# Optimization experiments

Hardware: AMD Instinct MI355X
Metric: run time of the kernel (lower is better)

## Reference

```python
import jax, jax.numpy as jnp
import numpy as np

DIM = 1024
HEADS = 16
HEAD_DIM = DIM // HEADS
HIDDEN = 4 * DIM
B, N = 2, 2048
LS_INIT = 1e-4


def _layernorm(x, w, b, eps=1e-5):
    mu = jnp.mean(x, axis=-1, keepdims=True)
    var = jnp.var(x, axis=-1, keepdims=True)
    return (x - mu) * jax.lax.rsqrt(var + eps) * w + b


def setup_inputs() -> dict:
    key = jax.random.key(0)
    ks = jax.random.split(key, 8)
    s = 0.02
    return {
        "x": jax.random.normal(ks[0], (B, N, DIM), jnp.float32),
        "ln1_w": jnp.ones((DIM,), jnp.float32),
        "ln1_b": jnp.zeros((DIM,), jnp.float32),
        "qkv_w": jax.random.normal(ks[1], (3 * DIM, DIM), jnp.float32) * s,
        "qkv_b": jnp.zeros((3 * DIM,), jnp.float32),
        "proj_w": jax.random.normal(ks[2], (DIM, DIM), jnp.float32) * s,
        "proj_b": jnp.zeros((DIM,), jnp.float32),
        "ls1_gamma": jnp.full((DIM,), LS_INIT, jnp.float32),
        "ln2_w": jnp.ones((DIM,), jnp.float32),
        "ln2_b": jnp.zeros((DIM,), jnp.float32),
        "fc1_w": jax.random.normal(ks[3], (HIDDEN, DIM), jnp.float32) * s,
        "fc1_b": jnp.zeros((HIDDEN,), jnp.float32),
        "fc2_w": jax.random.normal(ks[4], (DIM, HIDDEN), jnp.float32) * s,
        "fc2_b": jnp.zeros((DIM,), jnp.float32),
        "ls2_gamma": jnp.full((DIM,), LS_INIT, jnp.float32),
    }


def reference(x, ln1_w, ln1_b, qkv_w, qkv_b, proj_w, proj_b, ls1_gamma,
              ln2_w, ln2_b, fc1_w, fc1_b, fc2_w, fc2_b, ls2_gamma):
    Bn, Nn, C = x.shape
    scale = HEAD_DIM ** -0.5

    # --- attention branch (pre-norm) ---
    h = _layernorm(x, ln1_w, ln1_b)
    qkv = h @ qkv_w.T + qkv_b                      # [B,N,3C]
    qkv = qkv.reshape(Bn, Nn, 3, HEADS, HEAD_DIM)
    q = qkv[:, :, 0].transpose(0, 2, 1, 3)         # [B,H,N,D]
    k = qkv[:, :, 1].transpose(0, 2, 1, 3)
    v = qkv[:, :, 2].transpose(0, 2, 1, 3)
    attn = jnp.einsum('bhnd,bhmd->bhnm', q, k) * scale  # [B,H,N,N]
    attn = jax.nn.softmax(attn, axis=-1)
    o = jnp.einsum('bhnm,bhmd->bhnd', attn, v)
    o = o.transpose(0, 2, 1, 3).reshape(Bn, Nn, C)
    o = o @ proj_w.T + proj_b
    x = x + o * ls1_gamma

    # --- MLP branch (pre-norm) ---
    h = _layernorm(x, ln2_w, ln2_b)
    h = jax.nn.gelu(h @ fc1_w.T + fc1_b, approximate=False)
    h = h @ fc2_w.T + fc2_b
    x = x + h * ls2_gamma
    return x
```

## Files before the change

### kernel.cpp

```cpp
#include <hip/hip_runtime.h>

#define DIM 1024
#define HEADS 16
#define HEAD_DIM 64
#define HIDDEN 4096
#define BB 2
#define NN 2048
#define TOK (BB*NN)

typedef __attribute__((ext_vector_type(8))) short bf16x8;
typedef __attribute__((ext_vector_type(4))) float f32x4;
typedef __attribute__((ext_vector_type(2))) int i32x2;

__device__ inline short f2bf(float f) {
    unsigned u = __float_as_uint(f);
    unsigned r = (u + 0x7fff + ((u >> 16) & 1)) >> 16;
    return (short)r;
}

#define GLL16(g, l)                                                          \
    __builtin_amdgcn_global_load_lds(                                        \
        (const __attribute__((address_space(1))) void*)(g),                  \
        (__attribute__((address_space(3))) void*)(l), 16, 0, 0)

__global__ void cvt_kernel(const float* __restrict__ in, short* __restrict__ out, int n4) {
    int i = blockIdx.x * blockDim.x + threadIdx.x;
    int stride = gridDim.x * blockDim.x;
    for (; i < n4; i += stride) {
        float4 v = ((const float4*)in)[i];
        short4 o;
        o.x = f2bf(v.x); o.y = f2bf(v.y); o.z = f2bf(v.z); o.w = f2bf(v.w);
        ((short4*)out)[i] = o;
    }
}

__global__ __launch_bounds__(256) void ln_kernel(const float* __restrict__ x,
                                                 const float* __restrict__ w,
                                                 const float* __restrict__ b,
                                                 short* __restrict__ out) {
    const int row = blockIdx.x;
    const int t = threadIdx.x;
    float4 v = ((const float4*)(x + (long)row * DIM))[t];
    float s = v.x + v.y + v.z + v.w;
    float ss = v.x * v.x + v.y * v.y + v.z * v.z + v.w * v.w;
#pragma unroll
    for (int m = 1; m < 64; m <<= 1) {
        s += __shfl_xor(s, m);
        ss += __shfl_xor(ss, m);
    }
    __shared__ float rs[4], rss[4];
    int wv = t >> 6;
    if ((t & 63) == 0) { rs[wv] = s; rss[wv] = ss; }
    __syncthreads();
    s = rs[0] + rs[1] + rs[2] + rs[3];
    ss = rss[0] + rss[1] + rss[2] + rss[3];
    float mean = s * (1.f / DIM);
    float var = ss * (1.f / DIM) - mean * mean;
    float rstd = rsqrtf(var + 1e-5f);
    float4 wv4 = ((const float4*)w)[t];
    float4 bv4 = ((const float4*)b)[t];
    short4 o;
    o.x = f2bf((v.x - mean) * rstd * wv4.x + bv4.x);
    o.y = f2bf((v.y - mean) * rstd * wv4.y + bv4.y);
    o.z = f2bf((v.z - mean) * rstd * wv4.z + bv4.z);
    o.w = f2bf((v.w - mean) * rstd * wv4.w + bv4.w);
    ((short4*)(out + (long)row * DIM))[t] = o;
}

template <int EPI>
__global__ __launch_bounds__(256) void gemm_bt(const short* __restrict__ A,
                                               const short* __restrict__ Bt,
                                               const float* __restrict__ bias,
                                               const float* __restrict__ resid,
                                               const float* __restrict__ gamma,
                                               void* __restrict__ Cout,
                                               int M, int N, int K) {
    __shared__ __align__(16) short As[128 * 32];
    __shared__ __align__(16) short Bs[128 * 32];
    const int t = threadIdx.x;
    const int w = t >> 6, l = t & 63, lr = l & 15, lg = l >> 4;
    const int wr = w >> 1, wc = w & 1;
    const int rowBase = blockIdx.y * 128, colBase = blockIdx.x * 128;

    f32x4 acc[4][4];
#pragma unroll
    for (int m = 0; m < 4; m++)
#pragma unroll
        for (int n = 0; n < 4; n++) acc[m][n] = {0.f, 0.f, 0.f, 0.f};

    for (int k0 = 0; k0 < K; k0 += 32) {
        __syncthreads();
#pragma unroll
        for (int r = 0; r < 2; r++) {
            int c = r * 256 + t;
            int row = c >> 2, col = (c & 3) * 8;
            const short* ga = A + (long)(rowBase + row) * K + k0 + col;
            const short* gb = Bt + (long)(colBase + row) * K + k0 + col;
            int ldsoff = (r * 256 + w * 64) * 8;
            GLL16(ga, As + ldsoff);
            GLL16(gb, Bs + ldsoff);
        }
        __syncthreads();
        bf16x8 af[4], bfr[4];
#pragma unroll
        for (int m = 0; m < 4; m++)
            af[m] = *(const bf16x8*)&As[(wr * 64 + m * 16 + lr) * 32 + lg * 8];
#pragma unroll
        for (int n = 0; n < 4; n++)
            bfr[n] = *(const bf16x8*)&Bs[(wc * 64 + n * 16 + lr) * 32 + lg * 8];
#pragma unroll
        for (int m = 0; m < 4; m++)
#pragma unroll
            for (int n = 0; n < 4; n++)
                acc[m][n] = __builtin_amdgcn_mfma_f32_16x16x32_bf16(af[m], bfr[n], acc[m][n], 0, 0, 0);
    }

#pragma unroll
    for (int n = 0; n < 4; n++) {
        int col = colBase + wc * 64 + n * 16 + lr;
        float bs = bias[col];
        float gm = (EPI == 3) ? gamma[col] : 0.f;
#pragma unroll
        for (int m = 0; m < 4; m++) {
            int row0 = rowBase + wr * 64 + m * 16 + lg * 4;
#pragma unroll
            for (int j = 0; j < 4; j++) {
                int row = row0 + j;
                float v = acc[m][n][j] + bs;
                if (EPI == 1) { if (col < DIM) v *= 0.125f; }
                if (EPI == 2) { v = 0.5f * v * (1.f + erff(v * 0.70710678118f)); }
                if (EPI == 3) {
                    float o = resid[(long)row * N + col] + v * gm;
                    ((float*)Cout)[(long)row * N + col] = o;
                } else {
                    ((short*)Cout)[(long)row * N + col] = f2bf(v);
                }
            }
        }
    }
}

__global__ __launch_bounds__(256) void attn_kernel(const short* __restrict__ qkv,
                                                   short* __restrict__ out) {
    const int id = blockIdx.x;
    const int rank = (id & 7) * 128 + (id >> 3);
    const int bh = rank >> 5, qt = rank & 31;
    const int b = bh >> 4, h = bh & 15;
    const int t = threadIdx.x;
    const int w = t >> 6, l = t & 63, lr = l & 15, lg = l >> 4;

    __shared__ __align__(16) short Ks[2][4096];
    __shared__ __align__(16) short Vs[2][4096];
    __shared__ __align__(16) short Ps[4][1024];

    bf16x8 qf[2];
    {
        const int qtok = b * NN + qt * 64 + w * 16 + lr;
        const short* qp = qkv + (long)qtok * (3 * DIM) + h * HEAD_DIM;
        qf[0] = *(const bf16x8*)(qp + lg * 8);
        qf[1] = *(const bf16x8*)(qp + 32 + lg * 8);
    }

    bf16x8 ones;
#pragma unroll
    for (int i = 0; i < 8; i++) ones[i] = (short)0x3F80;

    f32x4 o[4];
#pragma unroll
    for (int dn = 0; dn < 4; dn++) o[dn] = {0.f, 0.f, 0.f, 0.f};
    float mrow[4] = {-1e30f, -1e30f, -1e30f, -1e30f};
    float lrow[4] = {0.f, 0.f, 0.f, 0.f};

    const long tokbase = (long)(b * NN) * (3 * DIM);

    auto stage = [&](int cb, int kv0) {
#pragma unroll
        for (int r = 0; r < 2; r++) {
            int L = r * 256 + t;
            int krow = L >> 3;
            int kcol = ((L & 7) * 8) ^ ((krow & 7) << 3);
            const short* gk = qkv + tokbase + (long)(kv0 + krow) * (3 * DIM) + DIM + h * HEAD_DIM + kcol;
            GLL16(gk, &Ks[cb][(r * 256 + w * 64) * 8]);
            int kv = ((L >> 5) << 2) | ((L >> 1) & 3);
            int d  = ((L >> 3) & 3) * 16 + (L & 1) * 8;
            const short* gv = qkv + tokbase + (long)(kv0 + kv) * (3 * DIM) + 2 * DIM + h * HEAD_DIM + d;
            GLL16(gv, &Vs[cb][(r * 256 + w * 64) * 8]);
        }
    };

    stage(0, 0);
    int cur = 0;

    for (int kvt = 0; kvt < NN / 64; kvt++) {
        __syncthreads();
        if (kvt + 1 < NN / 64) stage(cur ^ 1, (kvt + 1) * 64);

        const int kswz = (lr & 7) << 3;
        f32x4 s[4];
#pragma unroll
        for (int n = 0; n < 4; n++) {
            int rowoff = (n * 16 + lr) * 64;
            bf16x8 kf0 = *(const bf16x8*)&Ks[cur][rowoff + ((lg * 8) ^ kswz)];
            bf16x8 kf1 = *(const bf16x8*)&Ks[cur][rowoff + ((32 + lg * 8) ^ kswz)];
            s[n] = {0.f, 0.f, 0.f, 0.f};
            s[n] = __builtin_amdgcn_mfma_f32_16x16x32_bf16(qf[0], kf0, s[n], 0, 0, 0);
            s[n] = __builtin_amdgcn_mfma_f32_16x16x32_bf16(qf[1], kf1, s[n], 0, 0, 0);
        }

        float corr[4];
#pragma unroll
        for (int j = 0; j < 4; j++) {
            float mx = fmaxf(fmaxf(s[0][j], s[1][j]), fmaxf(s[2][j], s[3][j]));
#pragma unroll
            for (int msk = 1; msk < 16; msk <<= 1) mx = fmaxf(mx, __shfl_xor(mx, msk));
            float mnew = fmaxf(mrow[j], mx);
            corr[j] = __expf(mrow[j] - mnew);
            mrow[j] = mnew;
            int prow = lg * 4 + j;
            int pswz = (prow & 7) << 3;
#pragma unroll
            for (int n = 0; n < 4; n++) {
                float p = __expf(s[n][j] - mnew);
                Ps[w][prow * 64 + ((n * 16 + lr) ^ pswz)] = f2bf(p);
            }
#pragma unroll
            for (int dn = 0; dn < 4; dn++) o[dn][j] *= corr[j];
        }

        i32x2 vrlo[2][4], vrhi[2][4];
#pragma unroll
        for (int kb = 0; kb < 2; kb++)
#pragma unroll
            for (int dn = 0; dn < 4; dn++) {
                unsigned voff = (unsigned)(size_t)&Vs[cur][(kb * 8 + lg * 2) * 256 + dn * 64 + lr];
                asm volatile("ds_read_b64_tr_b16 %0, %2\n\t"
                             "ds_read_b64_tr_b16 %1, %2 offset:512"
                             : "=&v"(vrlo[kb][dn]), "=&v"(vrhi[kb][dn])
                             : "v"(voff));
            }
        asm volatile("s_waitcnt lgkmcnt(0)" ::: "memory");
        __builtin_amdgcn_sched_barrier(0);

        f32x4 lsum = {0.f, 0.f, 0.f, 0.f};
#pragma unroll
        for (int kb = 0; kb < 2; kb++) {
            bf16x8 pf = *(const bf16x8*)&Ps[w][lr * 64 + ((kb * 32 + lg * 8) ^ ((lr & 7) << 3))];
            lsum = __builtin_amdgcn_mfma_f32_16x16x32_bf16(pf, ones, lsum, 0, 0, 0);
#pragma unroll
            for (int dn = 0; dn < 4; dn++) {
                union { i32x2 p[2]; bf16x8 v; } u;
                u.p[0] = vrlo[kb][dn];
                u.p[1] = vrhi[kb][dn];
                o[dn] = __builtin_amdgcn_mfma_f32_16x16x32_bf16(pf, u.v, o[dn], 0, 0, 0);
            }
        }
#pragma unroll
        for (int j = 0; j < 4; j++) lrow[j] = lrow[j] * corr[j] + lsum[j];

        cur ^= 1;
    }

#pragma unroll
    for (int j = 0; j < 4; j++) {
        float inv = 1.f / lrow[j];
        long tok = b * NN + qt * 64 + w * 16 + lg * 4 + j;
#pragma unroll
        for (int dn = 0; dn < 4; dn++)
            out[tok * DIM + h * HEAD_DIM + dn * 16 + lr] = f2bf(o[dn][j] * inv);
    }
}

extern "C" void kernel_launch(void* const* d_in, const int* in_sizes, int n_in,
                              void* d_out, int out_size, void* d_ws, size_t ws_size,
                              hipStream_t stream) {
    const float* x       = (const float*)d_in[0];
    const float* ln1_w   = (const float*)d_in[1];
    const float* ln1_b   = (const float*)d_in[2];
    const float* qkv_w   = (const float*)d_in[3];
    const float* qkv_b   = (const float*)d_in[4];
    const float* proj_w  = (const float*)d_in[5];
    const float* proj_b  = (const float*)d_in[6];
    const float* ls1_g   = (const float*)d_in[7];
    const float* ln2_w   = (const float*)d_in[8];
    const float* ln2_b   = (const float*)d_in[9];
    const float* fc1_w   = (const float*)d_in[10];
    const float* fc1_b   = (const float*)d_in[11];
    const float* fc2_w   = (const float*)d_in[12];
    const float* fc2_b   = (const float*)d_in[13];
    const float* ls2_g   = (const float*)d_in[14];

    char* p = (char*)d_ws;
    short* wqkv   = (short*)p; p += (size_t)3 * DIM * DIM * 2;
    short* wproj  = (short*)p; p += (size_t)DIM * DIM * 2;
    short* wfc1   = (short*)p; p += (size_t)HIDDEN * DIM * 2;
    short* wfc2   = (short*)p; p += (size_t)DIM * HIDDEN * 2;
    short* h1     = (short*)p; p += (size_t)TOK * DIM * 2;
    short* qkvbuf = (short*)p; p += (size_t)TOK * 3 * DIM * 2;
    short* attno  = (short*)p; p += (size_t)TOK * DIM * 2;
    float* x2     = (float*)p; p += (size_t)TOK * DIM * 4;
    short* h2     = (short*)p; p += (size_t)TOK * DIM * 2;
    short* fc1o   = (short*)p; p += (size_t)TOK * HIDDEN * 2;

    {
        int n4;
        n4 = 3 * DIM * DIM / 4;
        cvt_kernel<<<dim3(2048), dim3(256), 0, stream>>>(qkv_w, wqkv, n4);
        n4 = DIM * DIM / 4;
        cvt_kernel<<<dim3(1024), dim3(256), 0, stream>>>(proj_w, wproj, n4);
        n4 = HIDDEN * DIM / 4;
        cvt_kernel<<<dim3(2048), dim3(256), 0, stream>>>(fc1_w, wfc1, n4);
        n4 = DIM * HIDDEN / 4;
        cvt_kernel<<<dim3(2048), dim3(256), 0, stream>>>(fc2_w, wfc2, n4);
    }

    ln_kernel<<<dim3(TOK), dim3(256), 0, stream>>>(x, ln1_w, ln1_b, h1);

    gemm_bt<1><<<dim3(3 * DIM / 128, TOK / 128), dim3(256), 0, stream>>>(
        h1, wqkv, qkv_b, nullptr, nullptr, qkvbuf, TOK, 3 * DIM, DIM);

    attn_kernel<<<dim3(NN / 64 * BB * HEADS), dim3(256), 0, stream>>>(qkvbuf, attno);

    gemm_bt<3><<<dim3(DIM / 128, TOK / 128), dim3(256), 0, stream>>>(
        attno, wproj, proj_b, x, ls1_g, x2, TOK, DIM, DIM);

    ln_kernel<<<dim3(TOK), dim3(256), 0, stream>>>(x2, ln2_w, ln2_b, h2);

    gemm_bt<2><<<dim3(HIDDEN / 128, TOK / 128), dim3(256), 0, stream>>>(
        h2, wfc1, fc1_b, nullptr, nullptr, fc1o, TOK, HIDDEN, DIM);

    gemm_bt<3><<<dim3(DIM / 128, TOK / 128), dim3(256), 0, stream>>>(
        fc1o, wfc2, fc2_b, x2, ls2_g, (float*)d_out, TOK, DIM, HIDDEN);
}
```

Measured before the change: 473.9 us.

## Add 256x256 8-wave pipelined GEMM for QKV and FC1 projections

Introduces a new GEMM kernel with 256x256 output tiles, 8 waves per block, a double-buffered split-half LDS staging scheme using direct global-to-LDS loads with XOR swizzle, and interleaved MFMA/LDS-read phases with priority hints. It also remaps block IDs for L2 locality. The QKV and FC1 GEMMs switch to it, which should cut global traffic per FLOP and hide load latency. In exchange it uses more registers and LDS per block and adds many barriers. The old kernel keeps only the residual epilogue path.

```diff
diff --git a/kernel.cpp b/kernel.cpp
--- a/kernel.cpp
+++ b/kernel.cpp
@@ -22,6 +22,10 @@
     __builtin_amdgcn_global_load_lds(                                        \
         (const __attribute__((address_space(1))) void*)(g),                  \
         (__attribute__((address_space(3))) void*)(l), 16, 0, 0)
+
+#define BARRIER() do { asm volatile("" ::: "memory");                        \
+    __builtin_amdgcn_s_barrier();                                            \
+    asm volatile("" ::: "memory"); } while (0)
 
 __global__ void cvt_kernel(const float* __restrict__ in, short* __restrict__ out, int n4) {
     int i = blockIdx.x * blockDim.x + threadIdx.x;
@@ -68,6 +72,148 @@
 }
 
 template <int EPI>
+__global__ __launch_bounds__(512, 2) void gemm8(const short* __restrict__ A,
+                                                const short* __restrict__ Bt,
+                                                const float* __restrict__ bias,
+                                                short* __restrict__ Cout,
+                                                int M, int N, int K, int nbx) {
+    __shared__ __align__(16) short As[2][2][128 * 64];
+    __shared__ __align__(16) short Bs[2][2][128 * 64];
+
+    const int t = threadIdx.x;
+    const int w = t >> 6, l = t & 63, lr = l & 15, lg = l >> 4;
+    const int wr = w >> 2, wc = w & 3;
+
+    const int nwg = gridDim.x;
+    const int id = blockIdx.x;
+    const int r = (id & 7) * (nwg >> 3) + (id >> 3);
+    const int by = r / nbx, bx = r % nbx;
+    const int rowBase = by * 256, colBase = bx * 256;
+
+    f32x4 acc[8][4];
+#pragma unroll
+    for (int m = 0; m < 8; m++)
+#pragma unroll
+        for (int n = 0; n < 4; n++) acc[m][n] = {0.f, 0.f, 0.f, 0.f};
+
+    bf16x8 afr[4][2];
+    bf16x8 bfr[4][2];
+
+    const int NT = K >> 6;
+    const int ITERS = NT >> 1;
+
+    auto stageA = [&](int buf, int h, int tile) {
+        const long k0 = (long)tile * 64;
+#pragma unroll
+        for (int j = 0; j < 2; j++) {
+            int L = j * 512 + t;
+            int p = L >> 3;
+            int grow = ((p >> 6) << 7) + (h << 6) + (p & 63);
+            int colS = ((L & 7) ^ (p & 7)) << 3;
+            const short* g = A + (long)(rowBase + grow) * K + k0 + colS;
+            GLL16(g, &As[buf][h][(j * 512 + w * 64) * 8]);
+        }
+    };
+    auto stageB = [&](int buf, int h, int tile) {
+        const long k0 = (long)tile * 64;
+#pragma unroll
+        for (int j = 0; j < 2; j++) {
+            int L = j * 512 + t;
+            int p = L >> 3;
+            int grow = ((p >> 5) << 6) + (h << 5) + (p & 31);
+            int colS = ((L & 7) ^ (p & 7)) << 3;
+            const short* g = Bt + (long)(colBase + grow) * K + k0 + colS;
+            GLL16(g, &Bs[buf][h][(j * 512 + w * 64) * 8]);
+        }
+    };
+    auto ldA = [&](int buf, int mh) {
+#pragma unroll
+        for (int mm = 0; mm < 4; mm++) {
+            int phys = wr * 64 + mm * 16 + lr;
+            int base = phys * 64, sw = (phys & 7) << 3;
+#pragma unroll
+            for (int ks = 0; ks < 2; ks++)
+                afr[mm][ks] = *(const bf16x8*)&As[buf][mh][base + ((ks * 32 + lg * 8) ^ sw)];
+        }
+    };
+    auto ldB = [&](int buf, int nh) {
+#pragma unroll
+        for (int nn = 0; nn < 2; nn++) {
+            int phys = wc * 32 + nn * 16 + lr;
+            int base = phys * 64, sw = (phys & 7) << 3;
+#pragma unroll
+            for (int ks = 0; ks < 2; ks++)
+                bfr[nh * 2 + nn][ks] = *(const bf16x8*)&Bs[buf][nh][base + ((ks * 32 + lg * 8) ^ sw)];
+        }
+    };
+    auto mfma16 = [&](int mh, int nh) {
+        __builtin_amdgcn_s_setprio(1);
+#pragma unroll
+        for (int ks = 0; ks < 2; ks++)
+#pragma unroll
+            for (int mm = 0; mm < 4; mm++)
+#pragma unroll
+                for (int nn = 0; nn < 2; nn++)
+                    acc[mh * 4 + mm][nh * 2 + nn] = __builtin_amdgcn_mfma_f32_16x16x32_bf16(
+                        afr[mm][ks], bfr[nh * 2 + nn][ks], acc[mh * 4 + mm][nh * 2 + nn], 0, 0, 0);
+        __builtin_amdgcn_s_setprio(0);
+    };
+
+    stageA(0, 0, 0); stageB(0, 0, 0);
+    stageA(0, 1, 0); stageB(0, 1, 0);
+    stageA(1, 0, 1); stageB(1, 0, 1);
+    asm volatile("s_waitcnt vmcnt(4)" ::: "memory");
+    BARRIER();
+
+    for (int i = 0; i < ITERS; i++) {
+        const bool more = (i < ITERS - 1);
+        ldA(0, 0); ldB(0, 0);
+        stageA(1, 1, 2 * i + 1);
+        BARRIER(); mfma16(0, 0); BARRIER();
+        ldB(0, 1);
+        stageB(1, 1, 2 * i + 1);
+        BARRIER(); mfma16(0, 1); BARRIER();
+        ldA(0, 1);
+        if (more) stageA(0, 0, 2 * i + 2);
+        BARRIER(); mfma16(1, 0); BARRIER();
+        if (more) { stageB(0, 0, 2 * i + 2);
+                    asm volatile("s_waitcnt vmcnt(4)" ::: "memory"); }
+        else      { asm volatile("s_waitcnt vmcnt(0)" ::: "memory"); }
+        BARRIER(); mfma16(1, 1); BARRIER();
+        ldA(1, 0); ldB(1, 0);
+        if (more) stageA(0, 1, 2 * i + 2);
+        BARRIER(); mfma16(0, 0); BARRIER();
+        ldB(1, 1);
+        if (more) stageB(0, 1, 2 * i + 2);
+        BARRIER(); mfma16(0, 1); BARRIER();
+        ldA(1, 1);
+        if (more) stageA(1, 0, 2 * i + 3);
+        BARRIER(); mfma16(1, 0); BARRIER();
+        if (more) { stageB(1, 0, 2 * i + 3);
+                    asm volatile("s_waitcnt vmcnt(4)" ::: "memory"); }
+        else      { asm volatile("s_waitcnt vmcnt(0)" ::: "memory"); }
+        BARRIER(); mfma16(1, 1); BARRIER();
+    }
+
+#pragma unroll
+    for (int n = 0; n < 4; n++) {
+        int col = colBase + wc * 64 + n * 16 + lr;
+        float bs = bias[col];
+#pragma unroll
+        for (int m = 0; m < 8; m++) {
+            int row0 = rowBase + wr * 128 + m * 16 + lg * 4;
+#pragma unroll
+            for (int j = 0; j < 4; j++) {
+                float v = acc[m][n][j] + bs;
+                if (EPI == 1) { if (col < DIM) v *= 0.125f; }
+                if (EPI == 2) { v = 0.5f * v * (1.f + erff(v * 0.70710678118f)); }
+                Cout[(long)(row0 + j) * N + col] = f2bf(v);
+            }
+        }
+    }
+}
+
+template <int EPI>
 __global__ __launch_bounds__(256) void gemm_bt(const short* __restrict__ A,
                                                const short* __restrict__ Bt,
                                                const float* __restrict__ bias,
@@ -127,8 +273,6 @@
             for (int j = 0; j < 4; j++) {
                 int row = row0 + j;
                 float v = acc[m][n][j] + bs;
-                if (EPI == 1) { if (col < DIM) v *= 0.125f; }
-                if (EPI == 2) { v = 0.5f * v * (1.f + erff(v * 0.70710678118f)); }
                 if (EPI == 3) {
                     float o = resid[(long)row * N + col] + v * gm;
                     ((float*)Cout)[(long)row * N + col] = o;
@@ -315,8 +459,8 @@
 
     ln_kernel<<<dim3(TOK), dim3(256), 0, stream>>>(x, ln1_w, ln1_b, h1);
 
-    gemm_bt<1><<<dim3(3 * DIM / 128, TOK / 128), dim3(256), 0, stream>>>(
-        h1, wqkv, qkv_b, nullptr, nullptr, qkvbuf, TOK, 3 * DIM, DIM);
+    gemm8<1><<<dim3(192), dim3(512), 0, stream>>>(h1, wqkv, qkv_b, qkvbuf,
+                                                  TOK, 3 * DIM, DIM, 12);
 
     attn_kernel<<<dim3(NN / 64 * BB * HEADS), dim3(256), 0, stream>>>(qkvbuf, attno);
 
@@ -325,8 +469,8 @@
 
     ln_kernel<<<dim3(TOK), dim3(256), 0, stream>>>(x2, ln2_w, ln2_b, h2);
 
-    gemm_bt<2><<<dim3(HIDDEN / 128, TOK / 128), dim3(256), 0, stream>>>(
-        h2, wfc1, fc1_b, nullptr, nullptr, fc1o, TOK, HIDDEN, DIM);
+    gemm8<2><<<dim3(256), dim3(512), 0, stream>>>(h2, wfc1, fc1_b, fc1o,
+                                                  TOK, HIDDEN, DIM, 16);
 
     gemm_bt<3><<<dim3(DIM / 128, TOK / 128), dim3(256), 0, stream>>>(
         fc1o, wfc2, fc2_b, x2, ls2_g, (float*)d_out, TOK, DIM, HIDDEN);
```

Result: no change. 468.5 us (-1.1%).

## Replace GEMM with 8-wave double-buffered swizzled kernel using larger tiles

Applied to the files above, without the earlier changes.

Replaces the 128x128, single-buffered, 256-thread GEMM with a 512-thread kernel using 256- or 128-row by 256-column tiles and a K step of 64. Global-to-LDS loads are double-buffered and interleaved with MFMA quarters, using explicit vmcnt waits, barriers and setprio. LDS columns are XOR-swizzled to avoid bank conflicts, and workgroup IDs are remapped to improve L2 locality. The aim is to hide memory latency and raise MFMA utilization, at the cost of higher LDS and register use and fewer, larger workgroups that may underfill the CUs on the smaller GEMMs.

```diff
diff --git a/kernel.cpp b/kernel.cpp
--- a/kernel.cpp
+++ b/kernel.cpp
@@ -22,6 +22,10 @@
     __builtin_amdgcn_global_load_lds(                                        \
         (const __attribute__((address_space(1))) void*)(g),                  \
         (__attribute__((address_space(3))) void*)(l), 16, 0, 0)
+
+#define BARRIER() do { asm volatile("" ::: "memory");                        \
+    __builtin_amdgcn_s_barrier();                                            \
+    asm volatile("" ::: "memory"); } while (0)
 
 __global__ void cvt_kernel(const float* __restrict__ in, short* __restrict__ out, int n4) {
     int i = blockIdx.x * blockDim.x + threadIdx.x;
@@ -67,52 +71,132 @@
     ((short4*)(out + (long)row * DIM))[t] = o;
 }
 
-template <int EPI>
-__global__ __launch_bounds__(256) void gemm_bt(const short* __restrict__ A,
-                                               const short* __restrict__ Bt,
-                                               const float* __restrict__ bias,
-                                               const float* __restrict__ resid,
-                                               const float* __restrict__ gamma,
-                                               void* __restrict__ Cout,
-                                               int M, int N, int K) {
-    __shared__ __align__(16) short As[128 * 32];
-    __shared__ __align__(16) short Bs[128 * 32];
+template <int EPI, int BM>
+__global__ __launch_bounds__(512, 2) void gemm8(const short* __restrict__ A,
+                                                const short* __restrict__ Bt,
+                                                const float* __restrict__ bias,
+                                                const float* __restrict__ resid,
+                                                const float* __restrict__ gamma,
+                                                void* __restrict__ Cout,
+                                                int M, int N, int K, int nbx) {
+    constexpr int ALOADS = BM / 64;
+    constexpr int MMP = BM / 64;
+    constexpr int AR = BM / 32;
+
+    __shared__ __align__(16) short As[2][BM * 64];
+    __shared__ __align__(16) short Bs[2][2][128 * 64];
+
     const int t = threadIdx.x;
     const int w = t >> 6, l = t & 63, lr = l & 15, lg = l >> 4;
-    const int wr = w >> 1, wc = w & 1;
-    const int rowBase = blockIdx.y * 128, colBase = blockIdx.x * 128;
-
-    f32x4 acc[4][4];
-#pragma unroll
-    for (int m = 0; m < 4; m++)
+    const int wr = w >> 2, wc = w & 3;
+
+    const int nwg = gridDim.x;
+    const int id = blockIdx.x;
+    const int r = (id & 7) * (nwg >> 3) + (id >> 3);
+    const int by = r / nbx, bx = r % nbx;
+    const int rowBase = by * BM, colBase = bx * 256;
+
+    f32x4 acc[AR][4];
+#pragma unroll
+    for (int m = 0; m < AR; m++)
 #pragma unroll
         for (int n = 0; n < 4; n++) acc[m][n] = {0.f, 0.f, 0.f, 0.f};
 
-    for (int k0 = 0; k0 < K; k0 += 32) {
-        __syncthreads();
-#pragma unroll
-        for (int r = 0; r < 2; r++) {
-            int c = r * 256 + t;
-            int row = c >> 2, col = (c & 3) * 8;
-            const short* ga = A + (long)(rowBase + row) * K + k0 + col;
-            const short* gb = Bt + (long)(colBase + row) * K + k0 + col;
-            int ldsoff = (r * 256 + w * 64) * 8;
-            GLL16(ga, As + ldsoff);
-            GLL16(gb, Bs + ldsoff);
-        }
-        __syncthreads();
-        bf16x8 af[4], bfr[4];
-#pragma unroll
-        for (int m = 0; m < 4; m++)
-            af[m] = *(const bf16x8*)&As[(wr * 64 + m * 16 + lr) * 32 + lg * 8];
-#pragma unroll
-        for (int n = 0; n < 4; n++)
-            bfr[n] = *(const bf16x8*)&Bs[(wc * 64 + n * 16 + lr) * 32 + lg * 8];
-#pragma unroll
-        for (int m = 0; m < 4; m++)
-#pragma unroll
-            for (int n = 0; n < 4; n++)
-                acc[m][n] = __builtin_amdgcn_mfma_f32_16x16x32_bf16(af[m], bfr[n], acc[m][n], 0, 0, 0);
+    bf16x8 afr[MMP][2];
+    bf16x8 bfr[4][2];
+
+    const int NT = K >> 6;
+    const int ITERS = NT >> 1;
+
+    auto stageA = [&](int buf, int tile) {
+        const long k0 = (long)tile * 64;
+#pragma unroll
+        for (int j = 0; j < ALOADS; j++) {
+            int L = j * 512 + t;
+            int p = L >> 3;
+            int colS = ((L & 7) ^ (p & 7)) << 3;
+            const short* g = A + (long)(rowBase + p) * K + k0 + colS;
+            GLL16(g, &As[buf][(j * 512 + w * 64) * 8]);
+        }
+    };
+    auto stageBh = [&](int buf, int h, int tile) {
+        const long k0 = (long)tile * 64;
+#pragma unroll
+        for (int j = 0; j < 2; j++) {
+            int L = j * 512 + t;
+            int p = L >> 3;
+            int gcol = ((p >> 5) << 6) + (h << 5) + (p & 31);
+            int colS = ((L & 7) ^ (p & 7)) << 3;
+            const short* g = Bt + (long)(colBase + gcol) * K + k0 + colS;
+            GLL16(g, &Bs[buf][h][(j * 512 + w * 64) * 8]);
+        }
+    };
+    auto ldA = [&](int buf, int mh) {
+#pragma unroll
+        for (int mm = 0; mm < MMP; mm++) {
+            int phys = wr * (BM / 2) + mh * (BM / 4) + mm * 16 + lr;
+            int base = phys * 64, sw = (phys & 7) << 3;
+#pragma unroll
+            for (int ks = 0; ks < 2; ks++)
+                afr[mm][ks] = *(const bf16x8*)&As[buf][base + ((ks * 32 + lg * 8) ^ sw)];
+        }
+    };
+    auto ldB = [&](int buf, int nh) {
+#pragma unroll
+        for (int nn = 0; nn < 2; nn++) {
+            int phys = wc * 32 + nn * 16 + lr;
+            int base = phys * 64, sw = (phys & 7) << 3;
+#pragma unroll
+            for (int ks = 0; ks < 2; ks++)
+                bfr[nh * 2 + nn][ks] = *(const bf16x8*)&Bs[buf][nh][base + ((ks * 32 + lg * 8) ^ sw)];
+        }
+    };
+    auto mfmaQ = [&](int mh, int nh) {
+        __builtin_amdgcn_s_setprio(1);
+#pragma unroll
+        for (int ks = 0; ks < 2; ks++)
+#pragma unroll
+            for (int mm = 0; mm < MMP; mm++)
+#pragma unroll
+                for (int nn = 0; nn < 2; nn++)
+                    acc[mh * MMP + mm][nh * 2 + nn] = __builtin_amdgcn_mfma_f32_16x16x32_bf16(
+                        afr[mm][ks], bfr[nh * 2 + nn][ks], acc[mh * MMP + mm][nh * 2 + nn], 0, 0, 0);
+        __builtin_amdgcn_s_setprio(0);
+    };
+    auto waitVM = [&]() {
+        if constexpr (BM == 256) asm volatile("s_waitcnt vmcnt(8)" ::: "memory");
+        else                     asm volatile("s_waitcnt vmcnt(6)" ::: "memory");
+    };
+
+    stageBh(0, 0, 0); stageBh(0, 1, 0); stageA(0, 0);
+    stageBh(1, 0, 1); stageBh(1, 1, 1); stageA(1, 1);
+    waitVM();
+    BARRIER();
+
+    for (int i = 0; i < ITERS; i++) {
+        const bool more = (i < ITERS - 1);
+        ldA(0, 0); ldB(0, 0);
+        BARRIER(); mfmaQ(0, 0); BARRIER();
+        ldB(0, 1);
+        if (more) stageBh(0, 0, 2 * i + 2);
+        BARRIER(); mfmaQ(0, 1); BARRIER();
+        ldA(0, 1);
+        if (more) stageBh(0, 1, 2 * i + 2);
+        BARRIER(); mfmaQ(1, 0); BARRIER();
+        if (more) { stageA(0, 2 * i + 2); waitVM(); }
+        else      { asm volatile("s_waitcnt vmcnt(0)" ::: "memory"); }
+        BARRIER(); mfmaQ(1, 1); BARRIER();
+        ldA(1, 0); ldB(1, 0);
+        BARRIER(); mfmaQ(0, 0); BARRIER();
+        ldB(1, 1);
+        if (more) stageBh(1, 0, 2 * i + 3);
+        BARRIER(); mfmaQ(0, 1); BARRIER();
+        ldA(1, 1);
+        if (more) stageBh(1, 1, 2 * i + 3);
+        BARRIER(); mfmaQ(1, 0); BARRIER();
+        if (more) { stageA(1, 2 * i + 3); waitVM(); }
+        else      { asm volatile("s_waitcnt vmcnt(0)" ::: "memory"); }
+        BARRIER(); mfmaQ(1, 1); BARRIER();
     }
 
 #pragma unroll
@@ -121,8 +205,8 @@
         float bs = bias[col];
         float gm = (EPI == 3) ? gamma[col] : 0.f;
 #pragma unroll
-        for (int m = 0; m < 4; m++) {
-            int row0 = rowBase + wr * 64 + m * 16 + lg * 4;
+        for (int m = 0; m < AR; m++) {
+            int row0 = rowBase + wr * (BM / 2) + m * 16 + lg * 4;
 #pragma unroll
             for (int j = 0; j < 4; j++) {
                 int row = row0 + j;
@@ -315,19 +399,19 @@
 
     ln_kernel<<<dim3(TOK), dim3(256), 0, stream>>>(x, ln1_w, ln1_b, h1);
 
-    gemm_bt<1><<<dim3(3 * DIM / 128, TOK / 128), dim3(256), 0, stream>>>(
-        h1, wqkv, qkv_b, nullptr, nullptr, qkvbuf, TOK, 3 * DIM, DIM);
+    gemm8<1, 256><<<dim3(192), dim3(512), 0, stream>>>(
+        h1, wqkv, qkv_b, nullptr, nullptr, qkvbuf, TOK, 3 * DIM, DIM, 12);
 
     attn_kernel<<<dim3(NN / 64 * BB * HEADS), dim3(256), 0, stream>>>(qkvbuf, attno);
 
-    gemm_bt<3><<<dim3(DIM / 128, TOK / 128), dim3(256), 0, stream>>>(
-        attno, wproj, proj_b, x, ls1_g, x2, TOK, DIM, DIM);
+    gemm8<3, 128><<<dim3(128), dim3(512), 0, stream>>>(
+        attno, wproj, proj_b, x, ls1_g, x2, TOK, DIM, DIM, 4);
 
     ln_kernel<<<dim3(TOK), dim3(256), 0, stream>>>(x2, ln2_w, ln2_b, h2);
 
-    gemm_bt<2><<<dim3(HIDDEN / 128, TOK / 128), dim3(256), 0, stream>>>(
-        h2, wfc1, fc1_b, nullptr, nullptr, fc1o, TOK, HIDDEN, DIM);
-
-    gemm_bt<3><<<dim3(DIM / 128, TOK / 128), dim3(256), 0, stream>>>(
-        fc1o, wfc2, fc2_b, x2, ls2_g, (float*)d_out, TOK, DIM, HIDDEN);
-}
+    gemm8<2, 256><<<dim3(256), dim3(512), 0, stream>>>(
+        h2, wfc1, fc1_b, nullptr, nullptr, fc1o, TOK, HIDDEN, DIM, 16);
+
+    gemm8<3, 128><<<dim3(128), dim3(512), 0, stream>>>(
+        fc1o, wfc2, fc2_b, x2, ls2_g, (float*)d_out, TOK, DIM, HIDDEN, 4);
+}
```

New measurement: 442.8 us. 6.5% less time.
